# Kernel optimization log

Measured on AMD Instinct MI355X. Metric: run time of the kernel, lower is better.

Reference implementation:

```python
import jax, jax.numpy as jnp
import numpy as np

B, L, D = 2, 2048, 1024
H, Z = 16, 64  # n_heads, head_dim


def setup_inputs() -> dict:
    key = jax.random.key(0)
    k1, k2, k3 = jax.random.split(key, 3)
    scale = 1.0 / np.sqrt(D)  # keep projections O(1) for numeric sanity
    x = jax.random.normal(k1, (B, L, D), dtype=jnp.float32)
    Wq = jax.random.normal(k2, (H, Z, D), dtype=jnp.float32) * scale
    Wk = jax.random.normal(k3, (H, Z, D), dtype=jnp.float32) * scale
    beta = jnp.ones((1,), dtype=jnp.float32) / jnp.sqrt(jnp.float32(Z))  # default beta = 1/sqrt(head_dim)
    return {"x": x, "Wq": Wq, "Wk": Wk, "beta": beta}


def _energy(x, Wq, Wk, beta):
    # x: (b, l, d); Wq/Wk: (h, z, d); beta: (1,)
    kp = jnp.einsum('bld,hzd->blhz', x, Wk)
    qp = jnp.einsum('bld,hzd->blhz', x, Wq)
    b0 = beta[0]
    # attention[b,h,q,k] = beta * <k_proj[b,q,h], q_proj[b,k,h]>  (faithful to original index order)
    att = b0 * jnp.einsum('bqhz,bkhz->bhqk', kp, qp)
    e = jax.nn.logsumexp(att, axis=-1)          # (b, h, q)
    e = e.sum(axis=-1).sum(axis=-1)             # (b,)
    return (-1.0 / b0) * e


def reference(x, Wq, Wk, beta):
    # value_and_grad: forward returns (energy, d(energy.sum)/dx)
    def esum(xx):
        return _energy(xx, Wq, Wk, beta).sum()
    en = _energy(x, Wq, Wk, beta)               # (b,)
    gx = jax.grad(esum)(x)                      # (b, l, d)
    return en, gx
```

## Files before the change

### kernel.cpp

```cpp
#include <hip/hip_runtime.h>
#include <math.h>

#define L 2048
#define D 1024
#define H 16
#define Z 64
#define HZ 1024

typedef __bf16 bf16x8 __attribute__((ext_vector_type(8)));
typedef float f32x4 __attribute__((ext_vector_type(4)));
typedef float f32x16 __attribute__((ext_vector_type(16)));

#if __has_builtin(__builtin_amdgcn_exp2f)
#define EXP2(x) __builtin_amdgcn_exp2f(x)
#else
#define EXP2(x) exp2f(x)
#endif

__device__ __forceinline__ void async_ld16(const void* g, void* l) {
  __builtin_amdgcn_global_load_lds(
      (const __attribute__((address_space(1))) uint32_t*)(uintptr_t)g,
      (__attribute__((address_space(3))) uint32_t*)(uint32_t)(uintptr_t)l,
      16, 0, 0);
}

template<int NPIECE>
__device__ __forceinline__ void stage_async(const __bf16* __restrict__ g,
                                            int gstride, char* lds, int tid) {
  const int l = tid & 63, w = tid >> 6;
#pragma unroll
  for (int it = 0; it < NPIECE; ++it) {
    const int region = it * 4 + w;
    const int r = ((region >> 1) << 4) + (l & 15);
    const int c = ((region & 1) << 2) + (l >> 4);
    async_ld16(g + (size_t)r * gstride + c * 8, lds + (region << 10));
  }
}

__device__ __forceinline__ bf16x8 rfrag(const char* lds, int row, int cc) {
  const int region = ((row >> 4) << 1) + (cc >> 2);
  const int slot = (row & 15) + ((cc & 3) << 4);
  return *(const bf16x8*)(lds + region * 1024 + slot * 16);
}

__global__ __launch_bounds__(256) void cvt_kernel(const float* __restrict__ s,
                                                  __bf16* __restrict__ d, int n4) {
  int i = blockIdx.x * 256 + threadIdx.x;
  if (i < n4) {
    float4 v = ((const float4*)s)[i];
    union { __bf16 h[4]; uint2 u; } o;
    o.h[0] = (__bf16)v.x; o.h[1] = (__bf16)v.y;
    o.h[2] = (__bf16)v.z; o.h[3] = (__bf16)v.w;
    ((uint2*)d)[i] = o.u;
  }
}

__global__ __launch_bounds__(256) void wt_kernel(
    const float* __restrict__ Wk, const float* __restrict__ Wq,
    __bf16* __restrict__ Wkb, __bf16* __restrict__ Wqb,
    __bf16* __restrict__ Wkt, __bf16* __restrict__ Wqt) {
  const float* W = blockIdx.z ? Wq : Wk;
  __bf16* Wb = blockIdx.z ? Wqb : Wkb;
  __bf16* Wt = blockIdx.z ? Wqt : Wkt;
  __shared__ __bf16 tile[64][65];
  const int r0 = blockIdx.y * 64, c0 = blockIdx.x * 64;
  const int c = threadIdx.x & 63, rb = threadIdx.x >> 6;
#pragma unroll
  for (int i = 0; i < 16; ++i) {
    int r = rb + i * 4;
    __bf16 v = (__bf16)W[(size_t)(r0 + r) * D + c0 + c];
    tile[r][c] = v;
    Wb[(size_t)(r0 + r) * D + c0 + c] = v;
  }
  __syncthreads();
#pragma unroll
  for (int i = 0; i < 16; ++i) {
    int r = rb + i * 4;
    Wt[(size_t)(c0 + r) * HZ + r0 + c] = tile[c][r];
  }
}

__device__ __forceinline__ int lperm(int mg) {
  const int off = mg & 15;
  return (mg & ~15) | (((off >> 2) & 1) << 3) | (((off >> 3) & 1) << 2);
}

__global__ __launch_bounds__(256, 2) void proj_kernel(
    const __bf16* __restrict__ xb, const __bf16* __restrict__ Wkb,
    const __bf16* __restrict__ Wqb, const float* __restrict__ beta_p,
    __bf16* __restrict__ kp, __bf16* __restrict__ qp,
    __bf16* __restrict__ kpt, __bf16* __restrict__ qpt) {
  const __bf16* __restrict__ Wb = blockIdx.z ? Wqb : Wkb;
  __bf16* __restrict__ outn = blockIdx.z ? qp : kp;
  __bf16* __restrict__ outt = blockIdx.z ? qpt : kpt;
  const int n0 = blockIdx.x * 128, m0 = blockIdx.y * 128;
  const int tid = threadIdx.x, l = tid & 63, w = tid >> 6;
  const int l31 = l & 31, hi = l >> 5;
  const int mh = w >> 1, nh = w & 1;
  const float ab = beta_p[0] * 1.44269504f;
  const float ssc = sqrtf(fabsf(ab));
  const float sc = blockIdx.z ? ssc : ((ab < 0.f) ? -ssc : ssc);
  __shared__ __align__(16) char sA[2][16384], sB[2][16384];

  f32x16 acc[2][2];
#pragma unroll
  for (int mi = 0; mi < 2; ++mi)
#pragma unroll
    for (int ni = 0; ni < 2; ++ni)
#pragma unroll
      for (int i = 0; i < 16; ++i) acc[mi][ni][i] = 0.f;

  const __bf16* __restrict__ Abase = xb + (size_t)m0 * D;
  const __bf16* __restrict__ Bbase = Wb + (size_t)n0 * D;
  stage_async<4>(Abase, D, sA[0], tid);
  stage_async<4>(Bbase, D, sB[0], tid);
  __syncthreads();

  for (int k = 0; k < 16; ++k) {
    const int cur = k & 1, nxt = cur ^ 1;
    if (k < 15) {
      stage_async<4>(Abase + (k + 1) * 64, D, sA[nxt], tid);
      stage_async<4>(Bbase + (k + 1) * 64, D, sB[nxt], tid);
    }
#pragma unroll
    for (int ks = 0; ks < 4; ++ks) {
      bf16x8 am[2], bn[2];
#pragma unroll
      for (int mi = 0; mi < 2; ++mi)
        am[mi] = rfrag(sA[cur], mh * 64 + mi * 32 + l31, 2 * ks + hi);
#pragma unroll
      for (int ni = 0; ni < 2; ++ni)
        bn[ni] = rfrag(sB[cur], nh * 64 + ni * 32 + l31, 2 * ks + hi);
#pragma unroll
      for (int mi = 0; mi < 2; ++mi)
#pragma unroll
        for (int ni = 0; ni < 2; ++ni)
          acc[mi][ni] = __builtin_amdgcn_mfma_f32_32x32x16_bf16(
              am[mi], bn[ni], acc[mi][ni], 0, 0, 0);
    }
    __syncthreads();
  }

  const int b = m0 >> 11;
  const int h = (n0 >> 6) + nh;
  const size_t bh = (size_t)b * H + h;
#pragma unroll
  for (int mi = 0; mi < 2; ++mi)
#pragma unroll
    for (int ni = 0; ni < 2; ++ni) {
      const int z = ni * 32 + l31;
#pragma unroll
      for (int rg = 0; rg < 4; ++rg) {
        const int mloc = mh * 64 + mi * 32 + 8 * rg + 4 * hi;
        const int mg = (m0 & (L - 1)) + mloc;
        union { __bf16 hh[4]; uint2 u; } pk;
#pragma unroll
        for (int j = 0; j < 4; ++j) {
          const float v = acc[mi][ni][4 * rg + j];
          pk.hh[j] = (__bf16)v;
          outn[(bh * L + mg + j) * Z + z] = (__bf16)(v * sc);
        }
        *(uint2*)(outt + (bh * Z + z) * L + lperm(mg)) = pk.u;
      }
    }
}

template<int MODE>
__global__ __launch_bounds__(256, 2) void grad_kernel(
    const __bf16* __restrict__ Rg, const __bf16* __restrict__ Sg,
    const __bf16* __restrict__ Tg,
    float* __restrict__ lse, __bf16* __restrict__ Gout,
    __bf16* __restrict__ kscale_t) {
  const int bid = blockIdx.x;
  const int slot = bid >> 3;
  const int bh = (bid & 7) * 4 + (slot >> 4);
  const int qt = slot & 15;
  const int tid = threadIdx.x, l = tid & 63, w = tid >> 6;
  const int l31 = l & 31, hi = l >> 5;
  const int q0 = qt * 128 + w * 32;
  __shared__ __align__(16) char sS[3][8192], sT[3][8192];

  bf16x8 bres[4];
#pragma unroll
  for (int ks = 0; ks < 4; ++ks)
    bres[ks] = *(const bf16x8*)(
        Rg + ((size_t)bh * L + q0 + l31) * Z + ks * 16 + hi * 8);

  f32x16 pv[2];
#pragma unroll
  for (int zt = 0; zt < 2; ++zt)
#pragma unroll
    for (int i = 0; i < 16; ++i) pv[zt][i] = 0.f;
  float li = 0.f;

  const __bf16* __restrict__ Sbase = Sg + (size_t)bh * L * Z;
  const __bf16* __restrict__ Tbase = Tg + (size_t)bh * Z * L;

  stage_async<2>(Sbase, Z, sS[0], tid);
  stage_async<2>(Tbase, L, sT[0], tid);
  stage_async<2>(Sbase + (size_t)64 * Z, Z, sS[1], tid);
  stage_async<2>(Tbase + 64, L, sT[1], tid);
  asm volatile("s_waitcnt vmcnt(4)" ::: "memory");
  __builtin_amdgcn_s_barrier();

  const char* s0 = sS[0]; const char* s1 = sS[1]; char* s2 = sS[2];
  const char* t0 = sT[0]; const char* t1 = sT[1]; char* t2 = sT[2];

  for (int kt = 0; kt < 32; ++kt) {
    bf16x8 av[8], bt[8];
#pragma unroll
    for (int ks = 0; ks < 4; ++ks) {
      av[ks]     = rfrag(s0, l31,      2 * ks + hi);
      av[4 + ks] = rfrag(s0, 32 + l31, 2 * ks + hi);
      bt[2 * ks]     = rfrag(t0, l31,      2 * ks + hi);
      bt[2 * ks + 1] = rfrag(t0, 32 + l31, 2 * ks + hi);
    }
    if (kt < 30) {
      stage_async<2>(Sbase + (size_t)(kt + 2) * 64 * Z, Z, s2, tid);
      stage_async<2>(Tbase + (kt + 2) * 64, L, t2, tid);
    }
    f32x16 st[2];
#pragma unroll
    for (int i = 0; i < 16; ++i) { st[0][i] = 0.f; st[1][i] = 0.f; }
    __builtin_amdgcn_s_setprio(1);
#pragma unroll
    for (int ks = 0; ks < 4; ++ks) {
      st[0] = __builtin_amdgcn_mfma_f32_32x32x16_bf16(av[ks], bres[ks], st[0], 0, 0, 0);
      st[1] = __builtin_amdgcn_mfma_f32_32x32x16_bf16(av[4 + ks], bres[ks], st[1], 0, 0, 0);
    }
    __builtin_amdgcn_s_setprio(0);
    uint32_t P32[2][8];
    float lsn = 0.f;
#pragma unroll
    for (int nt = 0; nt < 2; ++nt)
#pragma unroll
      for (int i = 0; i < 8; ++i) {
        float e0 = EXP2(st[nt][2 * i]);
        float e1 = EXP2(st[nt][2 * i + 1]);
        if (MODE == 0) lsn += e0 + e1;
        union { __bf16 hh[2]; uint32_t u; } pk;
        pk.hh[0] = (__bf16)e0; pk.hh[1] = (__bf16)e1;
        P32[nt][i] = pk.u;
      }
    if (MODE == 0) li += lsn;
    __builtin_amdgcn_s_setprio(1);
#pragma unroll
    for (int kc = 0; kc < 4; ++kc) {
      union { uint32_t u[4]; bf16x8 v; } a;
#pragma unroll
      for (int i = 0; i < 4; ++i) a.u[i] = P32[kc >> 1][4 * (kc & 1) + i];
      pv[0] = __builtin_amdgcn_mfma_f32_32x32x16_bf16(a.v, bt[2 * kc], pv[0], 0, 0, 0);
      pv[1] = __builtin_amdgcn_mfma_f32_32x32x16_bf16(a.v, bt[2 * kc + 1], pv[1], 0, 0, 0);
    }
    __builtin_amdgcn_s_setprio(0);
    if (kt < 30) {
      asm volatile("s_waitcnt vmcnt(4)" ::: "memory");
      __builtin_amdgcn_s_barrier();
    } else if (kt == 30) {
      asm volatile("s_waitcnt vmcnt(0)" ::: "memory");
      __builtin_amdgcn_s_barrier();
    }
    const char* x;
    x = s0; s0 = s1; s1 = s2; s2 = (char*)x;
    x = t0; t0 = t1; t1 = t2; t2 = (char*)x;
  }

  if (MODE == 0) li += __shfl_xor(li, 32);
  const int b = bh >> 4, head = bh & (H - 1);
#pragma unroll
  for (int r = 0; r < 16; ++r) {
    const int qoff = (r & 3) + 8 * (r >> 2) + 4 * hi;
    float scl = 1.f;
    if (MODE == 0)
      scl = 1.f / __int_as_float(
                __builtin_amdgcn_ds_bpermute(4 * qoff, __float_as_int(li)));
    const size_t orow = ((size_t)b * L + q0 + qoff) * HZ + head * Z;
    Gout[orow + l31]      = (__bf16)(-pv[0][r] * scl);
    Gout[orow + 32 + l31] = (__bf16)(-pv[1][r] * scl);
  }
  if (MODE == 0) {
    if (hi == 0)
      lse[(size_t)bh * L + q0 + l31] = __logf(li);
    const float rli = 1.f / li;
    const int pos4 = (l & 7) * 4;
    const int lb = lperm(pos4);
    float sf[4];
#pragma unroll
    for (int j = 0; j < 4; ++j)
      sf[j] = __int_as_float(
          __builtin_amdgcn_ds_bpermute(4 * (lb + j), __float_as_int(rli)));
    __bf16* krow = kscale_t + ((size_t)bh * Z + (l >> 3)) * L + q0 + pos4;
#pragma unroll
    for (int pass = 0; pass < 8; ++pass) {
      union { __bf16 hh[4]; uint2 u; } v;
      v.u = *(uint2*)krow;
      v.hh[0] = (__bf16)((float)v.hh[0] * sf[0]);
      v.hh[1] = (__bf16)((float)v.hh[1] * sf[1]);
      v.hh[2] = (__bf16)((float)v.hh[2] * sf[2]);
      v.hh[3] = (__bf16)((float)v.hh[3] * sf[3]);
      *(uint2*)krow = v.u;
      krow += (size_t)8 * L;
    }
  }
}

__global__ __launch_bounds__(256) void energy_kernel(
    const float* __restrict__ lse_ws, const float* __restrict__ beta_p,
    float* __restrict__ out) {
  const int b = blockIdx.x;
  const float* p = lse_ws + (size_t)b * H * L;
  float sum = 0.f;
  for (int i = threadIdx.x; i < H * L; i += 256) sum += p[i];
#pragma unroll
  for (int off = 1; off < 64; off <<= 1) sum += __shfl_xor(sum, off, 64);
  __shared__ float wsum[4];
  if ((threadIdx.x & 63) == 0) wsum[threadIdx.x >> 6] = sum;
  __syncthreads();
  if (threadIdx.x == 0)
    out[b] = -(wsum[0] + wsum[1] + wsum[2] + wsum[3]) / beta_p[0];
}

__global__ __launch_bounds__(256, 2) void gx_kernel(
    const __bf16* __restrict__ Gkp, const __bf16* __restrict__ Gqp,
    const __bf16* __restrict__ Wkt, const __bf16* __restrict__ Wqt,
    float* __restrict__ gx) {
  const int bid = blockIdx.x;
  const int xcd = bid & 7;
  const int nt_ = (bid >> 3) & 7;
  const int mg = bid >> 6;
  const int m0 = (xcd * 8 + mg) * 64;
  const int n0 = nt_ * 128;
  const int tid = threadIdx.x, l = tid & 63, w = tid >> 6;
  const int l31 = l & 31, hi = l >> 5;
  const int mh = w >> 1, nh = w & 1;
  __shared__ __align__(16) char sA[3][8192], sB[3][16384];

  f32x16 acc[2];
#pragma unroll
  for (int ni = 0; ni < 2; ++ni)
#pragma unroll
    for (int i = 0; i < 16; ++i) acc[ni][i] = 0.f;

  auto stageK = [&](int kn, char* a, char* b) {
    const __bf16* __restrict__ An = (kn < 16 ? Gkp : Gqp);
    const __bf16* __restrict__ Bn = (kn < 16 ? Wkt : Wqt);
    const int k0 = (kn & 15) * 64;
    stage_async<2>(An + (size_t)m0 * HZ + k0, HZ, a, tid);
    stage_async<4>(Bn + (size_t)n0 * HZ + k0, HZ, b, tid);
  };

  stageK(0, sA[0], sB[0]);
  stageK(1, sA[1], sB[1]);
  asm volatile("s_waitcnt vmcnt(6)" ::: "memory");
  __builtin_amdgcn_s_barrier();

  const char* a0 = sA[0]; const char* a1 = sA[1]; char* a2 = sA[2];
  const char* b0 = sB[0]; const char* b1 = sB[1]; char* b2 = sB[2];

  for (int kk = 0; kk < 32; ++kk) {
    if (kk < 30) stageK(kk + 2, a2, b2);
#pragma unroll
    for (int ks = 0; ks < 4; ++ks) {
      bf16x8 am, bn[2];
      am = rfrag(a0, mh * 32 + l31, 2 * ks + hi);
#pragma unroll
      for (int ni = 0; ni < 2; ++ni)
        bn[ni] = rfrag(b0, nh * 64 + ni * 32 + l31, 2 * ks + hi);
      __builtin_amdgcn_s_setprio(1);
#pragma unroll
      for (int ni = 0; ni < 2; ++ni)
        acc[ni] = __builtin_amdgcn_mfma_f32_32x32x16_bf16(
            am, bn[ni], acc[ni], 0, 0, 0);
      __builtin_amdgcn_s_setprio(0);
    }
    if (kk < 30) {
      asm volatile("s_waitcnt vmcnt(6)" ::: "memory");
      __builtin_amdgcn_s_barrier();
    } else if (kk == 30) {
      asm volatile("s_waitcnt vmcnt(0)" ::: "memory");
      __builtin_amdgcn_s_barrier();
    }
    const char* x;
    x = a0; a0 = a1; a1 = a2; a2 = (char*)x;
    x = b0; b0 = b1; b1 = b2; b2 = (char*)x;
  }
#pragma unroll
  for (int ni = 0; ni < 2; ++ni) {
    const int n = n0 + nh * 64 + ni * 32 + l31;
#pragma unroll
    for (int r = 0; r < 16; ++r) {
      const int m = m0 + mh * 32 + (r & 3) + 8 * (r >> 2) + 4 * hi;
      gx[(size_t)m * D + n] = acc[ni][r];
    }
  }
}

extern "C" void kernel_launch(void* const* d_in, const int* in_sizes, int n_in,
                              void* d_out, int out_size, void* d_ws, size_t ws_size,
                              hipStream_t stream) {
  const float* x    = (const float*)d_in[0];
  const float* Wq   = (const float*)d_in[1];
  const float* Wk   = (const float*)d_in[2];
  const float* beta = (const float*)d_in[3];
  float* out = (float*)d_out;

  char* ws = (char*)d_ws;
  __bf16* xb  = (__bf16*)(ws);
  __bf16* Wkb = (__bf16*)(ws + (8ull  << 20));
  __bf16* Wqb = (__bf16*)(ws + (10ull << 20));
  __bf16* Wkt = (__bf16*)(ws + (12ull << 20));
  __bf16* Wqt = (__bf16*)(ws + (14ull << 20));
  __bf16* kp  = (__bf16*)(ws + (16ull << 20));
  __bf16* qp  = (__bf16*)(ws + (24ull << 20));
  __bf16* kpt = (__bf16*)(ws + (32ull << 20));
  __bf16* qpt = (__bf16*)(ws + (40ull << 20));
  __bf16* Gkp = (__bf16*)(ws + (48ull << 20));
  __bf16* Gqp = (__bf16*)(ws + (56ull << 20));
  float*  lse = (float*)(ws + (64ull << 20));

  cvt_kernel<<<4096, 256, 0, stream>>>(x, xb, 1048576);
  wt_kernel<<<dim3(16, 16, 2), 256, 0, stream>>>(Wk, Wq, Wkb, Wqb, Wkt, Wqt);
  proj_kernel<<<dim3(8, 32, 2), 256, 0, stream>>>(xb, Wkb, Wqb, beta, kp, qp, kpt, qpt);
  grad_kernel<0><<<512, 256, 0, stream>>>(kp, qp, qpt, lse, Gkp, kpt);
  grad_kernel<1><<<512, 256, 0, stream>>>(qp, kp, kpt, lse, Gqp, kpt);
  energy_kernel<<<2, 256, 0, stream>>>(lse, beta, out);
  gx_kernel<<<512, 256, 0, stream>>>(Gkp, Gqp, Wkt, Wqt, out + 2);
}
```

Baseline: 280.1 us.

## Shrink projection tile to 64x128, triple-buffer LDS, remap blocks across XCDs

The projection GEMM now uses 64-row M tiles, which doubles the grid to 1024 blocks over a flattened, XCD-aware block index so that blocks sharing x rows land on the same XCD. The LDS pipeline goes from double to triple buffering with explicit vmcnt waits and raw barriers in place of __syncthreads, and MFMA issue is wrapped in s_setprio. The aim is better occupancy, load/compute overlap and L2 locality for the projection stage. The cost is lower MFMA reuse per block and more fragile hand-tuned wait counts.

```diff
diff --git a/kernel.cpp b/kernel.cpp
--- a/kernel.cpp
+++ b/kernel.cpp
@@ -90,79 +90,93 @@
     const __bf16* __restrict__ Wqb, const float* __restrict__ beta_p,
     __bf16* __restrict__ kp, __bf16* __restrict__ qp,
     __bf16* __restrict__ kpt, __bf16* __restrict__ qpt) {
-  const __bf16* __restrict__ Wb = blockIdx.z ? Wqb : Wkb;
-  __bf16* __restrict__ outn = blockIdx.z ? qp : kp;
-  __bf16* __restrict__ outt = blockIdx.z ? qpt : kpt;
-  const int n0 = blockIdx.x * 128, m0 = blockIdx.y * 128;
+  const int bid = blockIdx.x;
+  const int zf = bid >> 9;
+  const int xcd = bid & 7;
+  const int nt_ = (bid >> 3) & 7;
+  const int mg_ = (bid >> 6) & 7;
+  const int m0 = (xcd * 8 + mg_) * 64;
+  const int n0 = nt_ * 128;
+  const __bf16* __restrict__ Wb = zf ? Wqb : Wkb;
+  __bf16* __restrict__ outn = zf ? qp : kp;
+  __bf16* __restrict__ outt = zf ? qpt : kpt;
   const int tid = threadIdx.x, l = tid & 63, w = tid >> 6;
   const int l31 = l & 31, hi = l >> 5;
   const int mh = w >> 1, nh = w & 1;
   const float ab = beta_p[0] * 1.44269504f;
   const float ssc = sqrtf(fabsf(ab));
-  const float sc = blockIdx.z ? ssc : ((ab < 0.f) ? -ssc : ssc);
-  __shared__ __align__(16) char sA[2][16384], sB[2][16384];
-
-  f32x16 acc[2][2];
-#pragma unroll
-  for (int mi = 0; mi < 2; ++mi)
-#pragma unroll
-    for (int ni = 0; ni < 2; ++ni)
-#pragma unroll
-      for (int i = 0; i < 16; ++i) acc[mi][ni][i] = 0.f;
+  const float sc = zf ? ssc : ((ab < 0.f) ? -ssc : ssc);
+  __shared__ __align__(16) char sA[3][8192], sB[3][16384];
+
+  f32x16 acc[2];
+#pragma unroll
+  for (int ni = 0; ni < 2; ++ni)
+#pragma unroll
+    for (int i = 0; i < 16; ++i) acc[ni][i] = 0.f;
 
   const __bf16* __restrict__ Abase = xb + (size_t)m0 * D;
   const __bf16* __restrict__ Bbase = Wb + (size_t)n0 * D;
-  stage_async<4>(Abase, D, sA[0], tid);
-  stage_async<4>(Bbase, D, sB[0], tid);
-  __syncthreads();
-
-  for (int k = 0; k < 16; ++k) {
-    const int cur = k & 1, nxt = cur ^ 1;
-    if (k < 15) {
-      stage_async<4>(Abase + (k + 1) * 64, D, sA[nxt], tid);
-      stage_async<4>(Bbase + (k + 1) * 64, D, sB[nxt], tid);
-    }
+  auto stageK = [&](int kn, char* a, char* b) {
+    stage_async<2>(Abase + kn * 64, D, a, tid);
+    stage_async<4>(Bbase + kn * 64, D, b, tid);
+  };
+
+  stageK(0, sA[0], sB[0]);
+  stageK(1, sA[1], sB[1]);
+  asm volatile("s_waitcnt vmcnt(6)" ::: "memory");
+  __builtin_amdgcn_s_barrier();
+
+  const char* a0 = sA[0]; const char* a1 = sA[1]; char* a2 = sA[2];
+  const char* b0 = sB[0]; const char* b1 = sB[1]; char* b2 = sB[2];
+
+  for (int kk = 0; kk < 16; ++kk) {
+    if (kk < 14) stageK(kk + 2, a2, b2);
 #pragma unroll
     for (int ks = 0; ks < 4; ++ks) {
-      bf16x8 am[2], bn[2];
-#pragma unroll
-      for (int mi = 0; mi < 2; ++mi)
-        am[mi] = rfrag(sA[cur], mh * 64 + mi * 32 + l31, 2 * ks + hi);
+      bf16x8 am, bn[2];
+      am = rfrag(a0, mh * 32 + l31, 2 * ks + hi);
 #pragma unroll
       for (int ni = 0; ni < 2; ++ni)
-        bn[ni] = rfrag(sB[cur], nh * 64 + ni * 32 + l31, 2 * ks + hi);
-#pragma unroll
-      for (int mi = 0; mi < 2; ++mi)
-#pragma unroll
-        for (int ni = 0; ni < 2; ++ni)
-          acc[mi][ni] = __builtin_amdgcn_mfma_f32_32x32x16_bf16(
-              am[mi], bn[ni], acc[mi][ni], 0, 0, 0);
-    }
-    __syncthreads();
+        bn[ni] = rfrag(b0, nh * 64 + ni * 32 + l31, 2 * ks + hi);
+      __builtin_amdgcn_s_setprio(1);
+#pragma unroll
+      for (int ni = 0; ni < 2; ++ni)
+        acc[ni] = __builtin_amdgcn_mfma_f32_32x32x16_bf16(
+            am, bn[ni], acc[ni], 0, 0, 0);
+      __builtin_amdgcn_s_setprio(0);
+    }
+    if (kk < 14) {
+      asm volatile("s_waitcnt vmcnt(6)" ::: "memory");
+      __builtin_amdgcn_s_barrier();
+    } else if (kk == 14) {
+      asm volatile("s_waitcnt vmcnt(0)" ::: "memory");
+      __builtin_amdgcn_s_barrier();
+    }
+    const char* x;
+    x = a0; a0 = a1; a1 = a2; a2 = (char*)x;
+    x = b0; b0 = b1; b1 = b2; b2 = (char*)x;
   }
 
   const int b = m0 >> 11;
   const int h = (n0 >> 6) + nh;
   const size_t bh = (size_t)b * H + h;
 #pragma unroll
-  for (int mi = 0; mi < 2; ++mi)
-#pragma unroll
-    for (int ni = 0; ni < 2; ++ni) {
-      const int z = ni * 32 + l31;
-#pragma unroll
-      for (int rg = 0; rg < 4; ++rg) {
-        const int mloc = mh * 64 + mi * 32 + 8 * rg + 4 * hi;
-        const int mg = (m0 & (L - 1)) + mloc;
-        union { __bf16 hh[4]; uint2 u; } pk;
-#pragma unroll
-        for (int j = 0; j < 4; ++j) {
-          const float v = acc[mi][ni][4 * rg + j];
-          pk.hh[j] = (__bf16)v;
-          outn[(bh * L + mg + j) * Z + z] = (__bf16)(v * sc);
-        }
-        *(uint2*)(outt + (bh * Z + z) * L + lperm(mg)) = pk.u;
+  for (int ni = 0; ni < 2; ++ni) {
+    const int z = ni * 32 + l31;
+#pragma unroll
+    for (int rg = 0; rg < 4; ++rg) {
+      const int mloc = mh * 32 + 8 * rg + 4 * hi;
+      const int mg = (m0 & (L - 1)) + mloc;
+      union { __bf16 hh[4]; uint2 u; } pk;
+#pragma unroll
+      for (int j = 0; j < 4; ++j) {
+        const float v = acc[ni][4 * rg + j];
+        pk.hh[j] = (__bf16)v;
+        outn[(bh * L + mg + j) * Z + z] = (__bf16)(v * sc);
       }
-    }
+      *(uint2*)(outt + (bh * Z + z) * L + lperm(mg)) = pk.u;
+    }
+  }
 }
 
 template<int MODE>
@@ -420,7 +434,7 @@
 
   cvt_kernel<<<4096, 256, 0, stream>>>(x, xb, 1048576);
   wt_kernel<<<dim3(16, 16, 2), 256, 0, stream>>>(Wk, Wq, Wkb, Wqb, Wkt, Wqt);
-  proj_kernel<<<dim3(8, 32, 2), 256, 0, stream>>>(xb, Wkb, Wqb, beta, kp, qp, kpt, qpt);
+  proj_kernel<<<1024, 256, 0, stream>>>(xb, Wkb, Wqb, beta, kp, qp, kpt, qpt);
   grad_kernel<0><<<512, 256, 0, stream>>>(kp, qp, qpt, lse, Gkp, kpt);
   grad_kernel<1><<<512, 256, 0, stream>>>(qp, kp, kpt, lse, Gqp, kpt);
   energy_kernel<<<2, 256, 0, stream>>>(lse, beta, out);
```

New measurement: 290.1 us. +3.6%, slower.
